# Kernel optimization log

Measured on AMD Instinct MI355X. Metric: run time of the kernel, lower is better.

The kernel has to match this reference:

```python
import jax, jax.numpy as jnp
import numpy as np
from jax import lax

LN_LAMBDA = 2.0  # ln_lambda from init

def setup_inputs() -> dict:
    key = jax.random.key(0)
    k1, k2, k3 = jax.random.split(key, 3)
    x = jax.random.normal(k1, (32, 32, 256, 256), dtype=jnp.float32)
    w_bar = jax.random.normal(k2, (32, 32, 3, 3), dtype=jnp.float32) * 0.1
    bias = jax.random.normal(k3, (32,), dtype=jnp.float32) * 0.1
    return {"x": x, "w_bar": w_bar, "bias": bias}

def reference(x, w_bar, bias):
    # _update_u_v: full SVD of weight reshaped to [height, -1]; torch uses
    # w.view(h,-1).data, i.e. sigma is detached from the graph.
    h = w_bar.shape[0]
    w2d = lax.stop_gradient(w_bar).reshape(h, -1)  # [32, 288]
    s = jnp.linalg.svd(w2d, full_matrices=False, compute_uv=False)
    sigma = jnp.maximum(jnp.ones_like(s[0]), s[0] / LN_LAMBDA)
    w = w_bar / sigma  # rescaled weight used by wrapped module
    # wrapped module: Conv2d(32, 32, kernel_size=3, padding=1)
    out = lax.conv_general_dilated(
        x, w,
        window_strides=(1, 1),
        padding=((1, 1), (1, 1)),
        dimension_numbers=("NCHW", "OIHW", "NCHW"),
    )
    return out + bias.reshape(1, -1, 1, 1)
```

## Files before the change

kernel.cpp:

```cpp
#include <hip/hip_runtime.h>
#include <math.h>


typedef __attribute__((ext_vector_type(8))) __bf16 frag8;
typedef __attribute__((ext_vector_type(16))) float f32x16;
typedef __attribute__((ext_vector_type(8))) unsigned short u16x8;

__device__ __forceinline__ unsigned short bf16bits(float v) {
  __bf16 h = (__bf16)v;
  return __builtin_bit_cast(unsigned short, h);
}

__global__ __launch_bounds__(1024) void sn_prep_kernel(
    const float* __restrict__ w_bar,
    unsigned short* __restrict__ w_out)
{
  __shared__ __align__(16) float sw[9216];
  __shared__ __align__(16) float swT[9216];
  __shared__ float G0[1024];
  __shared__ float Gpp[2048];
  __shared__ float vvec[32];
  __shared__ float svec[32];
  __shared__ float scal[2];
  const int tid = threadIdx.x;

  for (int i = tid; i < 9216; i += 1024) {
    float v = w_bar[i];
    sw[i] = v;
    int k = i / 288;
    int t = i - k * 288;
    swT[t * 32 + k] = v;
  }
  __syncthreads();

  {
    const int i = tid >> 5, j = tid & 31;
    const float* ri = &sw[i * 288];
    float s0 = 0.f, s1 = 0.f;
    for (int t = 0; t < 288; t += 8) {
      float4 a = *(const float4*)(ri + t);
      float4 b = *(const float4*)(ri + t + 4);
      s0 = fmaf(a.x, swT[(t + 0) * 32 + j], s0);
      s0 = fmaf(a.y, swT[(t + 1) * 32 + j], s0);
      s0 = fmaf(a.z, swT[(t + 2) * 32 + j], s0);
      s0 = fmaf(a.w, swT[(t + 3) * 32 + j], s0);
      s1 = fmaf(b.x, swT[(t + 4) * 32 + j], s1);
      s1 = fmaf(b.y, swT[(t + 5) * 32 + j], s1);
      s1 = fmaf(b.z, swT[(t + 6) * 32 + j], s1);
      s1 = fmaf(b.w, swT[(t + 7) * 32 + j], s1);
    }
    G0[tid] = s0 + s1;
  }

  const float* src = G0;
  for (int sq = 0; sq < 6; ++sq) {
    float* dst = &Gpp[(sq & 1) * 1024];
    __syncthreads();
    {
      const int i = tid >> 5, j = tid & 31;
      float s0 = 0.f, s1 = 0.f;
#pragma unroll
      for (int t = 0; t < 32; t += 2) {
        s0 = fmaf(src[i * 32 + t], src[t * 32 + j], s0);
        s1 = fmaf(src[i * 32 + t + 1], src[(t + 1) * 32 + j], s1);
      }
      dst[tid] = s0 + s1;
    }
    __syncthreads();
    float s0 = dst[0];
    float inv = (s0 > 0.f) ? (1.f / s0) : 1.f;
    __syncthreads();
    dst[tid] *= inv;
    src = dst;
  }

  if (tid < 32) vvec[tid] = 1.f;
  __syncthreads();
  for (int it = 0; it < 4; ++it) {
    if (tid < 32) {
      float s = 0.f;
#pragma unroll
      for (int j = 0; j < 32; ++j) s = fmaf(src[tid * 32 + j], vvec[j], s);
      svec[tid] = s;
    }
    __syncthreads();
    if (tid == 0) {
      float n2 = 0.f;
      for (int j = 0; j < 32; ++j) n2 += svec[j] * svec[j];
      scal[0] = (n2 > 0.f) ? rsqrtf(n2) : 0.f;
    }
    __syncthreads();
    if (tid < 32) vvec[tid] = svec[tid] * scal[0];
    __syncthreads();
  }

  if (tid < 32) {
    float s = 0.f;
#pragma unroll
    for (int j = 0; j < 32; ++j) s = fmaf(G0[tid * 32 + j], vvec[j], s);
    svec[tid] = s * vvec[tid];
  }
  __syncthreads();
  if (tid == 0) {
    float lam = 0.f;
    for (int j = 0; j < 32; ++j) lam += svec[j];
    lam = fmaxf(lam, 0.f);
    float sigma = fmaxf(1.f, 0.5f * sqrtf(lam));
    scal[1] = 1.f / sigma;
  }
  __syncthreads();
  float inv_sigma = scal[1];
  for (int e = tid; e < 9216; e += 1024) {
    int q = e >> 10;
    int rem = e & 1023;
    int k = rem >> 5;
    int c = rem & 31;
    float w = sw[k * 288 + c * 9 + q] * inv_sigma;
    __bf16 hb = (__bf16)w;
    float lo = w - (float)hb;
    w_out[e] = __builtin_bit_cast(unsigned short, hb);
    w_out[9216 + e] = bf16bits(lo);
  }
}

__global__ __launch_bounds__(512, 4) void sn_conv_mfma(
    const float* __restrict__ x, const unsigned short* __restrict__ wsp,
    const float* __restrict__ bias, float* __restrict__ out)
{
  __shared__ __align__(16) unsigned short wH[10240];
  __shared__ __align__(16) unsigned short wL[10240];
  __shared__ __align__(16) unsigned short sxH[9792];
  __shared__ __align__(16) unsigned short sxL[9792];

  const int tid  = threadIdx.x;
  const int lane = tid & 63;
  const int wv   = tid >> 6;
  const int l31  = lane & 31;
  const int half = lane >> 5;
  const int n  = blockIdx.z;
  const int y0 = blockIdx.y * 16;
  const int x0 = blockIdx.x * 64;

  for (int i = tid; i < 1152; i += 512) {
    ((u16x8*)wH)[i] = ((const u16x8*)wsp)[i];
    ((u16x8*)wL)[i] = ((const u16x8*)(wsp + 9216))[i];
  }
  for (int i = tid; i < 1024; i += 512) {
    wH[9216 + i] = 0;
    wL[9216 + i] = 0;
  }

  const int kb = 4 * half;
  const float4 b0 = *(const float4*)&bias[kb];
  const float4 b1 = *(const float4*)&bias[kb + 8];
  const float4 b2 = *(const float4*)&bias[kb + 16];
  const float4 b3 = *(const float4*)&bias[kb + 24];
  f32x16 acc0;
  acc0[0] = b0.x; acc0[1] = b0.y; acc0[2]  = b0.z; acc0[3]  = b0.w;
  acc0[4] = b1.x; acc0[5] = b1.y; acc0[6]  = b1.z; acc0[7]  = b1.w;
  acc0[8] = b2.x; acc0[9] = b2.y; acc0[10] = b2.z; acc0[11] = b2.w;
  acc0[12] = b3.x; acc0[13] = b3.y; acc0[14] = b3.z; acc0[15] = b3.w;
  f32x16 acc1 = acc0, acc2 = acc0, acc3 = acc0;

  int offB[5];
#pragma unroll
  for (int p = 0; p < 5; ++p) {
    int q = 2 * p + half; if (q > 8) q = 8;
    int dy = q / 3;
    int dx = q - 3 * dy;
    offB[p] = (dy * 68 + dx) * 8;
  }

  const float* xn = x + (size_t)n * 32 * 65536;

  for (int cs = 0; cs < 4; ++cs) {
    const int c0 = cs * 8;
    __syncthreads();
    for (int idx = tid; idx < 18 * 66; idx += 512) {
      int r   = idx / 66;
      int col = idx - r * 66;
      int gy = y0 - 1 + r;
      int gx = x0 - 1 + col;
      bool ok = ((unsigned)gy < 256u) && ((unsigned)gx < 256u);
      const float* px = xn + (size_t)c0 * 65536 + gy * 256 + gx;
      u16x8 hv, lv;
#pragma unroll
      for (int cl = 0; cl < 8; ++cl) {
        float v = ok ? px[(size_t)cl * 65536] : 0.f;
        __bf16 hb = (__bf16)v;
        float rl = v - (float)hb;
        hv[cl] = __builtin_bit_cast(unsigned short, hb);
        lv[cl] = bf16bits(rl);
      }
      int d = (r * 68 + col) * 8;
      *(u16x8*)&sxH[d] = hv;
      *(u16x8*)&sxL[d] = lv;
    }
    __syncthreads();

    frag8 aH[5], aL[5];
#pragma unroll
    for (int p = 0; p < 5; ++p) {
      int qa = 2 * p + half;
      int d = qa * 1024 + l31 * 32 + c0;
      aH[p] = __builtin_bit_cast(frag8, *(const u16x8*)&wH[d]);
      aL[p] = __builtin_bit_cast(frag8, *(const u16x8*)&wL[d]);
    }

#define LOAD_B(BH, BL, TT)                                                       \
    frag8 BH[5], BL[5];                                                          \
    {                                                                            \
      const int r_o = wv * 2 + ((TT) >> 1);                                      \
      const int dbase = (r_o * 68 + ((TT) & 1) * 32 + l31) * 8;                  \
      _Pragma("unroll")                                                          \
      for (int p = 0; p < 5; ++p) {                                              \
        BH[p] = __builtin_bit_cast(frag8, *(const u16x8*)&sxH[dbase + offB[p]]); \
        BL[p] = __builtin_bit_cast(frag8, *(const u16x8*)&sxL[dbase + offB[p]]); \
      }                                                                          \
    }

    {
      LOAD_B(bH0, bL0, 0)
      LOAD_B(bH1, bL1, 1)
#pragma unroll
      for (int p = 0; p < 5; ++p) {
        acc0 = __builtin_amdgcn_mfma_f32_32x32x16_bf16(aH[p], bH0[p], acc0, 0, 0, 0);
        acc1 = __builtin_amdgcn_mfma_f32_32x32x16_bf16(aH[p], bH1[p], acc1, 0, 0, 0);
        acc0 = __builtin_amdgcn_mfma_f32_32x32x16_bf16(aL[p], bH0[p], acc0, 0, 0, 0);
        acc1 = __builtin_amdgcn_mfma_f32_32x32x16_bf16(aL[p], bH1[p], acc1, 0, 0, 0);
        acc0 = __builtin_amdgcn_mfma_f32_32x32x16_bf16(aH[p], bL0[p], acc0, 0, 0, 0);
        acc1 = __builtin_amdgcn_mfma_f32_32x32x16_bf16(aH[p], bL1[p], acc1, 0, 0, 0);
      }
    }
    {
      LOAD_B(bH2, bL2, 2)
      LOAD_B(bH3, bL3, 3)
#pragma unroll
      for (int p = 0; p < 5; ++p) {
        acc2 = __builtin_amdgcn_mfma_f32_32x32x16_bf16(aH[p], bH2[p], acc2, 0, 0, 0);
        acc3 = __builtin_amdgcn_mfma_f32_32x32x16_bf16(aH[p], bH3[p], acc3, 0, 0, 0);
        acc2 = __builtin_amdgcn_mfma_f32_32x32x16_bf16(aL[p], bH2[p], acc2, 0, 0, 0);
        acc3 = __builtin_amdgcn_mfma_f32_32x32x16_bf16(aL[p], bH3[p], acc3, 0, 0, 0);
        acc2 = __builtin_amdgcn_mfma_f32_32x32x16_bf16(aH[p], bL2[p], acc2, 0, 0, 0);
        acc3 = __builtin_amdgcn_mfma_f32_32x32x16_bf16(aH[p], bL3[p], acc3, 0, 0, 0);
      }
    }
#undef LOAD_B
  }

#define ST_TILE(ACC, TT)                                                        \
  {                                                                             \
    const int r_o = wv * 2 + ((TT) >> 1);                                       \
    const int gx = x0 + ((TT) & 1) * 32 + l31;                                  \
    float* op = out + ((size_t)n * 32 + kb) * 65536 + (y0 + r_o) * 256 + gx;    \
    _Pragma("unroll")                                                           \
    for (int reg = 0; reg < 16; ++reg) {                                        \
      int krel = (reg & 3) + 8 * (reg >> 2);                                    \
      op[(size_t)krel * 65536] = ACC[reg];                                      \
    }                                                                           \
  }

  ST_TILE(acc0, 0)
  ST_TILE(acc1, 1)
  ST_TILE(acc2, 2)
  ST_TILE(acc3, 3)
#undef ST_TILE
}

extern "C" void kernel_launch(void* const* d_in, const int* in_sizes, int n_in,
                              void* d_out, int out_size, void* d_ws, size_t ws_size,
                              hipStream_t stream) {
  (void)in_sizes; (void)n_in; (void)out_size; (void)ws_size;
  const float* x     = (const float*)d_in[0];
  const float* w_bar = (const float*)d_in[1];
  const float* bias  = (const float*)d_in[2];
  float* out = (float*)d_out;
  unsigned short* wS = (unsigned short*)d_ws;

  sn_prep_kernel<<<1, 1024, 0, stream>>>(w_bar, wS);
  dim3 grid(256 / 64, 256 / 16, 32);
  sn_conv_mfma<<<grid, 512, 0, stream>>>(x, wS, bias, out);
}
```

Measured before the change: 513.5 us.

## Shrink conv tile to 8x32 and load weight fragments directly from global

The conv block tile shrinks from 16x64 to 8x32 pixels with 256 threads, and each wave computes two 32-pixel tiles instead of four. Weight fragments are no longer staged in LDS; each wave reads its A fragments straight from global memory on every channel slice, which drops the large shared weight buffers and should raise occupancy. In exchange, halo overhead per output pixel grows (10x34 input for 8x32 output), and weights are re-read from global or L2 on every block and channel slice.

```diff
diff --git a/kernel.cpp b/kernel.cpp
--- a/kernel.cpp
+++ b/kernel.cpp
@@ -123,14 +123,12 @@
   }
 }
 
-__global__ __launch_bounds__(512, 4) void sn_conv_mfma(
+__global__ __launch_bounds__(256, 5) void sn_conv_mfma(
     const float* __restrict__ x, const unsigned short* __restrict__ wsp,
     const float* __restrict__ bias, float* __restrict__ out)
 {
-  __shared__ __align__(16) unsigned short wH[10240];
-  __shared__ __align__(16) unsigned short wL[10240];
-  __shared__ __align__(16) unsigned short sxH[9792];
-  __shared__ __align__(16) unsigned short sxL[9792];
+  __shared__ __align__(16) unsigned short sxH[2880];
+  __shared__ __align__(16) unsigned short sxL[2880];
 
   const int tid  = threadIdx.x;
   const int lane = tid & 63;
@@ -138,17 +136,8 @@
   const int l31  = lane & 31;
   const int half = lane >> 5;
   const int n  = blockIdx.z;
-  const int y0 = blockIdx.y * 16;
-  const int x0 = blockIdx.x * 64;
-
-  for (int i = tid; i < 1152; i += 512) {
-    ((u16x8*)wH)[i] = ((const u16x8*)wsp)[i];
-    ((u16x8*)wL)[i] = ((const u16x8*)(wsp + 9216))[i];
-  }
-  for (int i = tid; i < 1024; i += 512) {
-    wH[9216 + i] = 0;
-    wL[9216 + i] = 0;
-  }
+  const int y0 = blockIdx.y * 8;
+  const int x0 = blockIdx.x * 32;
 
   const int kb = 4 * half;
   const float4 b0 = *(const float4*)&bias[kb];
@@ -160,7 +149,7 @@
   acc0[4] = b1.x; acc0[5] = b1.y; acc0[6]  = b1.z; acc0[7]  = b1.w;
   acc0[8] = b2.x; acc0[9] = b2.y; acc0[10] = b2.z; acc0[11] = b2.w;
   acc0[12] = b3.x; acc0[13] = b3.y; acc0[14] = b3.z; acc0[15] = b3.w;
-  f32x16 acc1 = acc0, acc2 = acc0, acc3 = acc0;
+  f32x16 acc1 = acc0;
 
   int offB[5];
 #pragma unroll
@@ -168,7 +157,7 @@
     int q = 2 * p + half; if (q > 8) q = 8;
     int dy = q / 3;
     int dx = q - 3 * dy;
-    offB[p] = (dy * 68 + dx) * 8;
+    offB[p] = (dy * 36 + dx) * 8;
   }
 
   const float* xn = x + (size_t)n * 32 * 65536;
@@ -176,9 +165,26 @@
   for (int cs = 0; cs < 4; ++cs) {
     const int c0 = cs * 8;
     __syncthreads();
-    for (int idx = tid; idx < 18 * 66; idx += 512) {
-      int r   = idx / 66;
-      int col = idx - r * 66;
+
+    frag8 aH[5], aL[5];
+#pragma unroll
+    for (int p = 0; p < 5; ++p) {
+      int qa = 2 * p + half;
+      int qc = qa > 8 ? 8 : qa;
+      int off = qc * 1024 + l31 * 32 + c0;
+      u16x8 h = *(const u16x8*)&wsp[off];
+      u16x8 l = *(const u16x8*)&wsp[9216 + off];
+      if (qa == 9) {
+        h = (u16x8)(0);
+        l = (u16x8)(0);
+      }
+      aH[p] = __builtin_bit_cast(frag8, h);
+      aL[p] = __builtin_bit_cast(frag8, l);
+    }
+
+    for (int idx = tid; idx < 10 * 34; idx += 256) {
+      int r   = idx / 34;
+      int col = idx - r * 34;
       int gy = y0 - 1 + r;
       int gx = x0 - 1 + col;
       bool ok = ((unsigned)gy < 256u) && ((unsigned)gx < 256u);
@@ -192,66 +198,33 @@
         hv[cl] = __builtin_bit_cast(unsigned short, hb);
         lv[cl] = bf16bits(rl);
       }
-      int d = (r * 68 + col) * 8;
+      int d = (r * 36 + col) * 8;
       *(u16x8*)&sxH[d] = hv;
       *(u16x8*)&sxL[d] = lv;
     }
     __syncthreads();
 
-    frag8 aH[5], aL[5];
+    const int db0 = ((wv * 2 + 0) * 36 + l31) * 8;
+    const int db1 = ((wv * 2 + 1) * 36 + l31) * 8;
 #pragma unroll
     for (int p = 0; p < 5; ++p) {
-      int qa = 2 * p + half;
-      int d = qa * 1024 + l31 * 32 + c0;
-      aH[p] = __builtin_bit_cast(frag8, *(const u16x8*)&wH[d]);
-      aL[p] = __builtin_bit_cast(frag8, *(const u16x8*)&wL[d]);
-    }
-
-#define LOAD_B(BH, BL, TT)                                                       \
-    frag8 BH[5], BL[5];                                                          \
-    {                                                                            \
-      const int r_o = wv * 2 + ((TT) >> 1);                                      \
-      const int dbase = (r_o * 68 + ((TT) & 1) * 32 + l31) * 8;                  \
-      _Pragma("unroll")                                                          \
-      for (int p = 0; p < 5; ++p) {                                              \
-        BH[p] = __builtin_bit_cast(frag8, *(const u16x8*)&sxH[dbase + offB[p]]); \
-        BL[p] = __builtin_bit_cast(frag8, *(const u16x8*)&sxL[dbase + offB[p]]); \
-      }                                                                          \
-    }
-
-    {
-      LOAD_B(bH0, bL0, 0)
-      LOAD_B(bH1, bL1, 1)
-#pragma unroll
-      for (int p = 0; p < 5; ++p) {
-        acc0 = __builtin_amdgcn_mfma_f32_32x32x16_bf16(aH[p], bH0[p], acc0, 0, 0, 0);
-        acc1 = __builtin_amdgcn_mfma_f32_32x32x16_bf16(aH[p], bH1[p], acc1, 0, 0, 0);
-        acc0 = __builtin_amdgcn_mfma_f32_32x32x16_bf16(aL[p], bH0[p], acc0, 0, 0, 0);
-        acc1 = __builtin_amdgcn_mfma_f32_32x32x16_bf16(aL[p], bH1[p], acc1, 0, 0, 0);
-        acc0 = __builtin_amdgcn_mfma_f32_32x32x16_bf16(aH[p], bL0[p], acc0, 0, 0, 0);
-        acc1 = __builtin_amdgcn_mfma_f32_32x32x16_bf16(aH[p], bL1[p], acc1, 0, 0, 0);
-      }
-    }
-    {
-      LOAD_B(bH2, bL2, 2)
-      LOAD_B(bH3, bL3, 3)
-#pragma unroll
-      for (int p = 0; p < 5; ++p) {
-        acc2 = __builtin_amdgcn_mfma_f32_32x32x16_bf16(aH[p], bH2[p], acc2, 0, 0, 0);
-        acc3 = __builtin_amdgcn_mfma_f32_32x32x16_bf16(aH[p], bH3[p], acc3, 0, 0, 0);
-        acc2 = __builtin_amdgcn_mfma_f32_32x32x16_bf16(aL[p], bH2[p], acc2, 0, 0, 0);
-        acc3 = __builtin_amdgcn_mfma_f32_32x32x16_bf16(aL[p], bH3[p], acc3, 0, 0, 0);
-        acc2 = __builtin_amdgcn_mfma_f32_32x32x16_bf16(aH[p], bL2[p], acc2, 0, 0, 0);
-        acc3 = __builtin_amdgcn_mfma_f32_32x32x16_bf16(aH[p], bL3[p], acc3, 0, 0, 0);
-      }
-    }
-#undef LOAD_B
+      frag8 bH0 = __builtin_bit_cast(frag8, *(const u16x8*)&sxH[db0 + offB[p]]);
+      frag8 bH1 = __builtin_bit_cast(frag8, *(const u16x8*)&sxH[db1 + offB[p]]);
+      frag8 bL0 = __builtin_bit_cast(frag8, *(const u16x8*)&sxL[db0 + offB[p]]);
+      frag8 bL1 = __builtin_bit_cast(frag8, *(const u16x8*)&sxL[db1 + offB[p]]);
+      acc0 = __builtin_amdgcn_mfma_f32_32x32x16_bf16(aH[p], bH0, acc0, 0, 0, 0);
+      acc1 = __builtin_amdgcn_mfma_f32_32x32x16_bf16(aH[p], bH1, acc1, 0, 0, 0);
+      acc0 = __builtin_amdgcn_mfma_f32_32x32x16_bf16(aL[p], bH0, acc0, 0, 0, 0);
+      acc1 = __builtin_amdgcn_mfma_f32_32x32x16_bf16(aL[p], bH1, acc1, 0, 0, 0);
+      acc0 = __builtin_amdgcn_mfma_f32_32x32x16_bf16(aH[p], bL0, acc0, 0, 0, 0);
+      acc1 = __builtin_amdgcn_mfma_f32_32x32x16_bf16(aH[p], bL1, acc1, 0, 0, 0);
+    }
   }
 
 #define ST_TILE(ACC, TT)                                                        \
   {                                                                             \
-    const int r_o = wv * 2 + ((TT) >> 1);                                       \
-    const int gx = x0 + ((TT) & 1) * 32 + l31;                                  \
+    const int r_o = wv * 2 + (TT);                                              \
+    const int gx = x0 + l31;                                                    \
     float* op = out + ((size_t)n * 32 + kb) * 65536 + (y0 + r_o) * 256 + gx;    \
     _Pragma("unroll")                                                           \
     for (int reg = 0; reg < 16; ++reg) {                                        \
@@ -262,8 +235,6 @@
 
   ST_TILE(acc0, 0)
   ST_TILE(acc1, 1)
-  ST_TILE(acc2, 2)
-  ST_TILE(acc3, 3)
 #undef ST_TILE
 }
 
@@ -278,6 +249,6 @@
   unsigned short* wS = (unsigned short*)d_ws;
 
   sn_prep_kernel<<<1, 1024, 0, stream>>>(w_bar, wS);
-  dim3 grid(256 / 64, 256 / 16, 32);
-  sn_conv_mfma<<<grid, 512, 0, stream>>>(x, wS, bias, out);
-}
+  dim3 grid(256 / 32, 256 / 8, 32);
+  sn_conv_mfma<<<grid, 256, 0, stream>>>(x, wS, bias, out);
+}
```

New measurement: 630.3 us. 22.8% more time.
